# Optimization experiments

Measured on AMD Instinct MI355X. Metric: run time of the kernel, lower is better.

The kernel has to match this reference:

```python
import jax, jax.numpy as jnp
import numpy as np

H, KV, D = 12, 4, 128  # n_head, n_kv_head, head_dim
VE_GATE_CH = 12

def _rmsnorm(x):
    eps = jnp.finfo(x.dtype).eps  # matches torch F.rms_norm default eps
    return x * jax.lax.rsqrt(jnp.mean(x * x, axis=-1, keepdims=True) + eps)

def _rope(x, cos, sin):
    d = x.shape[-1] // 2
    x1, x2 = x[..., :d], x[..., d:]
    return jnp.concatenate([x1 * cos + x2 * sin, -x1 * sin + x2 * cos], axis=-1)

def setup_inputs() -> dict:
    key = jax.random.key(0)
    ks = jax.random.split(key, 9)
    B, T, C = 2, 2048, 1536
    x = jax.random.normal(ks[0], (B, T, C), jnp.float32)
    ve = jax.random.normal(ks[1], (B, T, KV * D), jnp.float32)
    ang = jax.random.uniform(ks[2], (1, T, 1, D // 2), jnp.float32) * (2.0 * np.pi)
    cos, sin = jnp.cos(ang), jnp.sin(ang)
    Wq = jax.random.normal(ks[3], (H * D, C), jnp.float32) * 0.02
    Wk = jax.random.normal(ks[4], (KV * D, C), jnp.float32) * 0.02
    Wv = jax.random.normal(ks[5], (KV * D, C), jnp.float32) * 0.02
    Wproj = jax.random.normal(ks[6], (C, C), jnp.float32) * 0.02
    Wg = jax.random.normal(ks[7], (KV, VE_GATE_CH), jnp.float32) * 0.02
    return dict(x=x, ve=ve, cos=cos, sin=sin, Wq=Wq, Wk=Wk, Wv=Wv, Wproj=Wproj, Wg=Wg, window=1024)

def reference(x, ve, cos, sin, Wq, Wk, Wv, Wproj, Wg, window):
    B, T, C = x.shape
    q = (x @ Wq.T).reshape(B, T, H, D)
    k = (x @ Wk.T).reshape(B, T, KV, D)
    v = (x @ Wv.T).reshape(B, T, KV, D)
    # value-embedding gate: 3*sigmoid(Linear(x[..., :12])) per kv head
    gate = 3.0 * jax.nn.sigmoid(x[..., :VE_GATE_CH] @ Wg.T)  # [B,T,KV]
    v = v + gate[..., None] * ve.reshape(B, T, KV, D)
    q = _rmsnorm(_rope(q, cos, sin)) * 1.2
    k = _rmsnorm(_rope(k, cos, sin)) * 1.2
    rep = H // KV  # GQA group size
    qh = q.transpose(0, 2, 1, 3).reshape(B, KV, rep, T, D)
    kh = k.transpose(0, 2, 1, 3)  # [B,KV,T,D]
    vh = v.transpose(0, 2, 1, 3)
    scores = jnp.einsum('bgrtd,bgsd->bgrts', qh, kh) / np.sqrt(D)
    row = jnp.arange(T)[:, None]
    col = jnp.arange(T)[None, :]
    if window < 0 or window >= T:
        mask = col <= row  # pure causal
    else:
        mask = (col <= row) & (row - col <= window)  # causal sliding window
    scores = jnp.where(mask, scores, -jnp.inf)
    att = jax.nn.softmax(scores, axis=-1)
    y = jnp.einsum('bgrts,bgsd->bgrtd', att, vh)
    y = y.reshape(B, H, T, D).transpose(0, 2, 1, 3).reshape(B, T, H * D)
    return y @ Wproj.T
```

## Files before the change

kernel.cpp:

```cpp
#include <hip/hip_runtime.h>
#include <hip/hip_bf16.h>
#include <math.h>

#define B_  2
#define T_  2048
#define C_  1536
#define H_  12
#define KV_ 4
#define D_  128
#define M_  (B_*T_)
#define REP_ (H_/KV_)
#define NQKV_ 2560

typedef __bf16 bf16x8 __attribute__((ext_vector_type(8)));
typedef float  f32x4  __attribute__((ext_vector_type(4)));
typedef unsigned u32x4 __attribute__((ext_vector_type(4)));

union BCast { u32x4 u; bf16x8 b; };

__device__ inline bf16x8 ldb8(const ushort* p) {
    BCast c; c.u = *reinterpret_cast<const u32x4*>(p); return c.b;
}

__device__ inline ushort f2bf(float f) {
    union { float f; unsigned u; } v; v.f = f;
    unsigned u = v.u;
    return (ushort)((u + 0x7FFF + ((u >> 16) & 1)) >> 16);
}

__device__ inline float bf2f(ushort u) {
    union { unsigned u; float f; } v; v.u = (unsigned)u << 16;
    return v.f;
}

__device__ inline void async_copy16(const ushort* g, ushort* l) {
    __builtin_amdgcn_global_load_lds(
        (const __attribute__((address_space(1))) unsigned*)g,
        (__attribute__((address_space(3))) unsigned*)l, 16, 0, 0);
}

template<bool BF16OUT>
__global__ __launch_bounds__(256) void gemm_bf16_bt(const ushort* __restrict__ A,
                                                    const ushort* __restrict__ Bm,
                                                    void* __restrict__ Cp,
                                                    int M, int N, int K) {
    __shared__ ushort As[128 * 32];
    __shared__ ushort Bs[128 * 32];
    const int tid  = threadIdx.x;
    const int wave = tid >> 6, lane = tid & 63;
    const int m16 = lane & 15, quad = lane >> 4;
    const int bm = blockIdx.y * 128, bn = blockIdx.x * 128;
    const int wm = (wave >> 1) * 64, wn = (wave & 1) * 64;

    const int lrow = lane >> 2;
    const int lcol = (lane & 3) * 8;
    const ushort* Ag = A  + (size_t)(bm + wave * 16 + lrow) * K + lcol;
    const ushort* Bg = Bm + (size_t)(bn + wave * 16 + lrow) * K + lcol;
    ushort* AsW0 = As + wave * 512;
    ushort* AsW1 = As + 2048 + wave * 512;
    ushort* BsW0 = Bs + wave * 512;
    ushort* BsW1 = Bs + 2048 + wave * 512;
    const size_t rowskip = (size_t)64 * K;

    f32x4 acc[4][4];
    #pragma unroll
    for (int i = 0; i < 4; i++)
        #pragma unroll
        for (int j = 0; j < 4; j++) acc[i][j] = (f32x4){0.f, 0.f, 0.f, 0.f};

    for (int k0 = 0; k0 < K; k0 += 32) {
        async_copy16(Ag + k0,           AsW0);
        async_copy16(Ag + k0 + rowskip, AsW1);
        async_copy16(Bg + k0,           BsW0);
        async_copy16(Bg + k0 + rowskip, BsW1);
        __syncthreads();

        bf16x8 af[4], bfr[4];
        #pragma unroll
        for (int i = 0; i < 4; i++)
            af[i] = ldb8(As + (wm + i * 16 + m16) * 32 + quad * 8);
        #pragma unroll
        for (int j = 0; j < 4; j++)
            bfr[j] = ldb8(Bs + (wn + j * 16 + m16) * 32 + quad * 8);
        #pragma unroll
        for (int i = 0; i < 4; i++)
            #pragma unroll
            for (int j = 0; j < 4; j++)
                acc[i][j] = __builtin_amdgcn_mfma_f32_16x16x32_bf16(af[i], bfr[j], acc[i][j], 0, 0, 0);
        __syncthreads();
    }

    #pragma unroll
    for (int i = 0; i < 4; i++) {
        #pragma unroll
        for (int reg = 0; reg < 4; reg++) {
            const int row = bm + wm + i * 16 + quad * 4 + reg;
            if constexpr (BF16OUT) {
                ushort* C = (ushort*)Cp;
                #pragma unroll
                for (int j = 0; j < 4; j++)
                    C[(size_t)row * N + bn + wn + j * 16 + m16] = f2bf(acc[i][j][reg]);
            } else {
                float* C = (float*)Cp;
                #pragma unroll
                for (int j = 0; j < 4; j++)
                    C[(size_t)row * N + bn + wn + j * 16 + m16] = acc[i][j][reg];
            }
        }
    }
}

#define SEG0 1572864
#define SEG1 2162688
#define SEG2 2359296
#define SEG3 2555904
#define SEG4 3145728
__global__ __launch_bounds__(256) void cast_all(const float* __restrict__ x,
                                                const float* __restrict__ Wq,
                                                const float* __restrict__ Wk,
                                                const float* __restrict__ Wv,
                                                const float* __restrict__ Wp,
                                                ushort* __restrict__ xb,
                                                ushort* __restrict__ Wqkvb,
                                                ushort* __restrict__ Wpb) {
    const int i = blockIdx.x * 256 + threadIdx.x;
    const float* src; ushort* dst; int off;
    if (i < SEG0)      { src = x;  dst = xb;                          off = 0; }
    else if (i < SEG1) { src = Wq; dst = Wqkvb;                       off = SEG0; }
    else if (i < SEG2) { src = Wk; dst = Wqkvb + (size_t)1536 * C_;   off = SEG1; }
    else if (i < SEG3) { src = Wv; dst = Wqkvb + (size_t)2048 * C_;   off = SEG2; }
    else               { src = Wp; dst = Wpb;                         off = SEG3; }
    const int j = i - off;
    float4 v = ((const float4*)src)[j];
    ((ushort4*)dst)[j] = make_ushort4(f2bf(v.x), f2bf(v.y), f2bf(v.z), f2bf(v.w));
}

__global__ __launch_bounds__(256) void rope_rms_cast(const ushort* __restrict__ qk,
                                                     ushort* __restrict__ outp,
                                                     const float* __restrict__ cosb,
                                                     const float* __restrict__ sinb,
                                                     int nh, int rowstride, int colbase,
                                                     float outscale) {
    const int idx = blockIdx.x * 4 + (threadIdx.x >> 6);
    const int bt = idx / nh;
    const int h  = idx - bt * nh;
    const int b  = bt >> 11;
    const int t  = bt & (T_ - 1);
    const ushort* p = qk + (size_t)bt * rowstride + colbase + h * D_;
    const int i = threadIdx.x & 63;
    const float x1 = bf2f(p[i]), x2 = bf2f(p[i + 64]);
    const float c = cosb[t * 64 + i], s = sinb[t * 64 + i];
    const float o1 =  x1 * c + x2 * s;
    const float o2 = -x1 * s + x2 * c;
    float ss = o1 * o1 + o2 * o2;
    #pragma unroll
    for (int off = 32; off > 0; off >>= 1) ss += __shfl_down(ss, off);
    ss = __shfl(ss, 0);
    const float scale = rsqrtf(ss * (1.0f / 128.0f) + 1.1920928955078125e-07f) * outscale;
    ushort* op = outp + ((size_t)(b * nh + h) * T_ + t) * D_;
    op[i]      = f2bf(o1 * scale);
    op[i + 64] = f2bf(o2 * scale);
}

__global__ __launch_bounds__(256) void gate_vt(const ushort* __restrict__ qkv,
                                               const float* __restrict__ x,
                                               const float* __restrict__ ve,
                                               const float* __restrict__ Wg,
                                               ushort* __restrict__ Vt) {
    const int t0 = blockIdx.x * 64, g = blockIdx.y, b = blockIdx.z;
    __shared__ float gateS[64];
    __shared__ ushort tile[128][66];
    const int tid = threadIdx.x;
    if (tid < 64) {
        const float* xr = x + (size_t)(b * T_ + t0 + tid) * C_;
        float acc = 0.f;
        #pragma unroll
        for (int c = 0; c < 12; c++) acc += xr[c] * Wg[g * 12 + c];
        gateS[tid] = 3.0f / (1.0f + __expf(-acc));
    }
    __syncthreads();
    #pragma unroll
    for (int i = 0; i < 32; i++) {
        int idx = i * 256 + tid;
        int r = idx >> 7;
        int d = idx & 127;
        size_t offv = (size_t)(b * T_ + t0 + r) * NQKV_ + 2048 + g * D_ + d;
        size_t offe = (size_t)(b * T_ + t0 + r) * 512   + g * D_ + d;
        tile[d][r] = f2bf(bf2f(qkv[offv]) + gateS[r] * ve[offe]);
    }
    __syncthreads();
    ushort* ob = Vt + ((size_t)(b * KV_ + g) * D_) * T_ + t0;
    #pragma unroll
    for (int i = 0; i < 32; i++) {
        int idx = i * 256 + tid;
        int d = idx >> 6;
        int c = idx & 63;
        ob[(size_t)d * T_ + c] = tile[d][c];
    }
}

__global__ __launch_bounds__(256, 3) void attn_mfma(const ushort* __restrict__ Qp,
                                                    const ushort* __restrict__ Kp,
                                                    const ushort* __restrict__ Vt,
                                                    ushort* __restrict__ Y,
                                                    const int* __restrict__ wptr) {
    const int t0 = blockIdx.x * 64;
    const int h  = blockIdx.y, b = blockIdx.z;
    const int g  = h / REP_;
    const int tid  = threadIdx.x;
    const int wave = tid >> 6, lane = tid & 63;
    const int m16 = lane & 15, quad = lane >> 4;

    __shared__ ushort Ks[4 * 32 * 32];
    __shared__ ushort Vs[128 * 32];
    __shared__ ushort Pl[4][16 * 40];

    const int w = *wptr;
    const bool windowed = (w >= 0 && w < T_);
    const unsigned wu = windowed ? (unsigned)w : 0x7FFFFFFFu;
    int s_lo = 0;
    if (windowed) { s_lo = t0 - w; if (s_lo < 0) s_lo = 0; }
    const int s_hi = t0 + 63;
    const int ss0 = s_lo & ~31;
    const int tw = t0 + wave * 16;

    const ushort* qrow = Qp + ((size_t)(b * H_ + h) * T_ + tw + m16) * D_ + quad * 8;
    bf16x8 qa[4];
    #pragma unroll
    for (int kc = 0; kc < 4; kc++) qa[kc] = ldb8(qrow + kc * 32);

    const ushort* kbase = Kp + (size_t)(b * KV_ + g) * T_ * D_;
    const ushort* vbase = Vt + (size_t)(b * KV_ + g) * D_ * T_;

    const int c0 = wave, c1 = wave + 4;
    const ushort* kg0 = kbase + (size_t)((c0 & 1) * 16 + (lane >> 2)) * D_ + (c0 >> 1) * 32 + (lane & 3) * 8;
    const ushort* kg1 = kbase + (size_t)((c1 & 1) * 16 + (lane >> 2)) * D_ + (c1 >> 1) * 32 + (lane & 3) * 8;
    ushort* kl0 = Ks + c0 * 512;
    ushort* kl1 = Ks + c1 * 512;
    const ushort* vg0 = vbase + (size_t)(c0 * 16 + (lane >> 2)) * T_ + (lane & 3) * 8;
    const ushort* vg1 = vbase + (size_t)(c1 * 16 + (lane >> 2)) * T_ + (lane & 3) * 8;
    ushort* vl0 = Vs + c0 * 512;
    ushort* vl1 = Vs + c1 * 512;

    f32x4 o[8];
    #pragma unroll
    for (int dt = 0; dt < 8; dt++) o[dt] = (f32x4){0.f, 0.f, 0.f, 0.f};
    f32x4 lacc = (f32x4){0.f, 0.f, 0.f, 0.f};
    BCast onesc; onesc.u = (u32x4){0x3F803F80u, 0x3F803F80u, 0x3F803F80u, 0x3F803F80u};
    const bf16x8 ones = onesc.b;
    ushort* pw = &Pl[wave][0];

    for (int ss = ss0; ss <= s_hi; ss += 32) {
        const size_t koff = (size_t)ss * D_;
        async_copy16(kg0 + koff, kl0);
        async_copy16(kg1 + koff, kl1);
        async_copy16(vg0 + ss,   vl0);
        async_copy16(vg1 + ss,   vl1);
        __syncthreads();

        f32x4 s0 = (f32x4){0.f,0.f,0.f,0.f};
        f32x4 s1 = (f32x4){0.f,0.f,0.f,0.f};
        #pragma unroll
        for (int kc = 0; kc < 4; kc++) {
            bf16x8 kf0 = ldb8(Ks + kc * 1024 + m16 * 32 + quad * 8);
            bf16x8 kf1 = ldb8(Ks + kc * 1024 + (16 + m16) * 32 + quad * 8);
            s0 = __builtin_amdgcn_mfma_f32_16x16x32_bf16(qa[kc], kf0, s0, 0, 0, 0);
            s1 = __builtin_amdgcn_mfma_f32_16x16x32_bf16(qa[kc], kf1, s1, 0, 0, 0);
        }

        const int sA = ss + m16, sB = ss + 16 + m16;
        #pragma unroll
        for (int reg = 0; reg < 4; reg++) {
            const int t = tw + quad * 4 + reg;
            const float pa = ((unsigned)(t - sA) <= wu) ? __expf(s0[reg]) : 0.f;
            const float pb = ((unsigned)(t - sB) <= wu) ? __expf(s1[reg]) : 0.f;
            pw[(quad * 4 + reg) * 40 + m16]      = f2bf(pa);
            pw[(quad * 4 + reg) * 40 + 16 + m16] = f2bf(pb);
        }

        __builtin_amdgcn_s_waitcnt(0xc07f);
        bf16x8 pfrag = ldb8(pw + m16 * 40 + quad * 8);

        #pragma unroll
        for (int dt = 0; dt < 8; dt++) {
            bf16x8 vf = ldb8(Vs + (dt * 16 + m16) * 32 + quad * 8);
            o[dt] = __builtin_amdgcn_mfma_f32_16x16x32_bf16(pfrag, vf, o[dt], 0, 0, 0);
        }
        lacc = __builtin_amdgcn_mfma_f32_16x16x32_bf16(pfrag, ones, lacc, 0, 0, 0);
        __syncthreads();
    }

    float inv[4];
    #pragma unroll
    for (int reg = 0; reg < 4; reg++) inv[reg] = 1.0f / lacc[reg];
    ushort* yb = Y + ((size_t)(b * T_ + tw + quad * 4) * H_ + h) * D_ + m16;
    #pragma unroll
    for (int reg = 0; reg < 4; reg++)
        #pragma unroll
        for (int dt = 0; dt < 8; dt++)
            yb[(size_t)reg * H_ * D_ + dt * 16] = f2bf(o[dt][reg] * inv[reg]);
}

extern "C" void kernel_launch(void* const* d_in, const int* in_sizes, int n_in,
                              void* d_out, int out_size, void* d_ws, size_t ws_size,
                              hipStream_t stream) {
    const float* x     = (const float*)d_in[0];
    const float* ve    = (const float*)d_in[1];
    const float* cosb  = (const float*)d_in[2];
    const float* sinb  = (const float*)d_in[3];
    const float* Wq    = (const float*)d_in[4];
    const float* Wk    = (const float*)d_in[5];
    const float* Wv    = (const float*)d_in[6];
    const float* Wproj = (const float*)d_in[7];
    const float* Wg    = (const float*)d_in[8];
    const int*   wptr  = (const int*)d_in[9];
    float* out = (float*)d_out;

    ushort* xb    = (ushort*)d_ws;
    ushort* qkv   = xb    + (size_t)M_ * C_;
    ushort* Qp    = qkv   + (size_t)M_ * NQKV_;
    ushort* Kp    = Qp    + (size_t)M_ * C_;
    ushort* Vt    = Kp    + (size_t)M_ * 512;
    ushort* Wqkvb = Vt    + (size_t)M_ * 512;
    ushort* Wpb   = Wqkvb + (size_t)NQKV_ * C_;

    cast_all<<<SEG4 / 256, 256, 0, stream>>>(x, Wq, Wk, Wv, Wproj, xb, Wqkvb, Wpb);

    gemm_bf16_bt<true><<<dim3(NQKV_ / 128, M_ / 128), 256, 0, stream>>>(xb, Wqkvb, qkv, M_, NQKV_, C_);

    gate_vt<<<dim3(T_ / 64, KV_, B_), 256, 0, stream>>>(qkv, x, ve, Wg, Vt);

    rope_rms_cast<<<M_ * H_ / 4, 256, 0, stream>>>(qkv, Qp, cosb, sinb, H_, NQKV_, 0,
                                                   1.2f * 1.2f * 0.08838834764831845f);
    rope_rms_cast<<<M_ * KV_ / 4, 256, 0, stream>>>(qkv, Kp, cosb, sinb, KV_, NQKV_, 1536, 1.0f);

    ushort* yb16 = qkv;
    attn_mfma<<<dim3(T_ / 64, H_, B_), 256, 0, stream>>>(Qp, Kp, Vt, yb16, wptr);

    gemm_bf16_bt<false><<<dim3(C_ / 128, M_ / 128), 256, 0, stream>>>(yb16, Wpb, out, M_, C_, C_);
}
```

Before: 285.5 us.

## Fuse RoPE and RMSNorm into QKV GEMM epilogue via permuted weight rows

```diff
diff --git a/kernel.cpp b/kernel.cpp
--- a/kernel.cpp
+++ b/kernel.cpp
@@ -37,6 +37,10 @@
     __builtin_amdgcn_global_load_lds(
         (const __attribute__((address_space(1))) unsigned*)g,
         (__attribute__((address_space(3))) unsigned*)l, 16, 0, 0);
+}
+
+__device__ __host__ inline int dperm(int d) {
+    return (d < 32) ? d : (d < 64 ? d + 32 : (d < 96 ? d - 32 : d));
 }
 
 template<bool BF16OUT>
@@ -110,11 +114,140 @@
     }
 }
 
+#define KQ_ 1536
+__global__ __launch_bounds__(256) void gemm_qkv(const ushort* __restrict__ A,
+                                                const ushort* __restrict__ Bm,
+                                                ushort* __restrict__ Qp,
+                                                ushort* __restrict__ Kp,
+                                                ushort* __restrict__ vbuf,
+                                                const float* __restrict__ cosb,
+                                                const float* __restrict__ sinb) {
+    __shared__ ushort As[128 * 32];
+    __shared__ ushort Bs[128 * 32];
+    const int tid  = threadIdx.x;
+    const int wave = tid >> 6, lane = tid & 63;
+    const int m16 = lane & 15, quad = lane >> 4;
+    const int bm = blockIdx.y * 128, bn = blockIdx.x * 128;
+    const int wm = (wave >> 1) * 64, wn = (wave & 1) * 64;
+
+    const int lrow = lane >> 2;
+    const int lcol = (lane & 3) * 8;
+    const ushort* Ag = A  + (size_t)(bm + wave * 16 + lrow) * KQ_ + lcol;
+    const ushort* Bg = Bm + (size_t)(bn + wave * 16 + lrow) * KQ_ + lcol;
+    ushort* AsW0 = As + wave * 512;
+    ushort* AsW1 = As + 2048 + wave * 512;
+    ushort* BsW0 = Bs + wave * 512;
+    ushort* BsW1 = Bs + 2048 + wave * 512;
+    const size_t rowskip = (size_t)64 * KQ_;
+
+    f32x4 acc[4][4];
+    #pragma unroll
+    for (int i = 0; i < 4; i++)
+        #pragma unroll
+        for (int j = 0; j < 4; j++) acc[i][j] = (f32x4){0.f, 0.f, 0.f, 0.f};
+
+    for (int k0 = 0; k0 < KQ_; k0 += 32) {
+        async_copy16(Ag + k0,           AsW0);
+        async_copy16(Ag + k0 + rowskip, AsW1);
+        async_copy16(Bg + k0,           BsW0);
+        async_copy16(Bg + k0 + rowskip, BsW1);
+        __syncthreads();
+
+        bf16x8 af[4], bfr[4];
+        #pragma unroll
+        for (int i = 0; i < 4; i++)
+            af[i] = ldb8(As + (wm + i * 16 + m16) * 32 + quad * 8);
+        #pragma unroll
+        for (int j = 0; j < 4; j++)
+            bfr[j] = ldb8(Bs + (wn + j * 16 + m16) * 32 + quad * 8);
+        #pragma unroll
+        for (int i = 0; i < 4; i++)
+            #pragma unroll
+            for (int j = 0; j < 4; j++)
+                acc[i][j] = __builtin_amdgcn_mfma_f32_16x16x32_bf16(af[i], bfr[j], acc[i][j], 0, 0, 0);
+        __syncthreads();
+    }
+
+    if (bn < 2048) {
+        float* ssqS = (float*)As;
+        float ssq[4][4];
+        #pragma unroll
+        for (int i = 0; i < 4; i++) {
+            #pragma unroll
+            for (int reg = 0; reg < 4; reg++) {
+                float v = acc[i][0][reg]*acc[i][0][reg] + acc[i][1][reg]*acc[i][1][reg]
+                        + acc[i][2][reg]*acc[i][2][reg] + acc[i][3][reg]*acc[i][3][reg];
+                v += __shfl_xor(v, 1); v += __shfl_xor(v, 2);
+                v += __shfl_xor(v, 4); v += __shfl_xor(v, 8);
+                ssq[i][reg] = v;
+            }
+        }
+        if (m16 == 0) {
+            #pragma unroll
+            for (int i = 0; i < 4; i++)
+                #pragma unroll
+                for (int reg = 0; reg < 4; reg++)
+                    ssqS[(wm + i*16 + quad*4 + reg) * 2 + (wave & 1)] = ssq[i][reg];
+        }
+        __syncthreads();
+
+        const bool isq = (bn < 1536);
+        const float osc = isq ? (1.2f * 1.2f * 0.08838834764831845f) : 1.0f;
+        const int hh  = isq ? (bn >> 7) : ((bn - 1536) >> 7);
+        const int nh  = isq ? H_ : KV_;
+        ushort* outp  = isq ? Qp : Kp;
+
+        float scl[4][4];
+        #pragma unroll
+        for (int i = 0; i < 4; i++) {
+            #pragma unroll
+            for (int reg = 0; reg < 4; reg++) {
+                const int r = wm + i*16 + quad*4 + reg;
+                const float tot = ssqS[r*2] + ssqS[r*2 + 1];
+                scl[i][reg] = rsqrtf(tot * (1.0f/128.0f) + 1.1920928955078125e-07f) * osc;
+            }
+        }
+
+        #pragma unroll
+        for (int i = 0; i < 4; i++) {
+            #pragma unroll
+            for (int reg = 0; reg < 4; reg++) {
+                const int row = bm + wm + i*16 + quad*4 + reg;
+                const int b = row >> 11, t = row & (T_ - 1);
+                ushort* orow = outp + ((size_t)(b * nh + hh) * T_ + t) * D_;
+                const float sc = scl[i][reg];
+                #pragma unroll
+                for (int jp = 0; jp < 2; jp++) {
+                    const int ipair = (wn ? 32 : 0) + jp*16 + m16;
+                    const float c = cosb[t*64 + ipair], s = sinb[t*64 + ipair];
+                    const float x1 = acc[i][jp][reg], x2 = acc[i][jp+2][reg];
+                    orow[wn + jp*16 + m16]       = f2bf((x1*c + x2*s) * sc);
+                    orow[wn + (jp+2)*16 + m16]   = f2bf((x2*c - x1*s) * sc);
+                }
+            }
+        }
+    } else {
+        const int cb = bn - 2048 + wn;
+        #pragma unroll
+        for (int i = 0; i < 4; i++) {
+            #pragma unroll
+            for (int reg = 0; reg < 4; reg++) {
+                const int row = bm + wm + i*16 + quad*4 + reg;
+                ushort* vr = vbuf + (size_t)row * 512 + cb + m16;
+                #pragma unroll
+                for (int j = 0; j < 4; j++)
+                    vr[j*16] = f2bf(acc[i][j][reg]);
+            }
+        }
+    }
+}
+
 #define SEG0 1572864
 #define SEG1 2162688
 #define SEG2 2359296
 #define SEG3 2555904
 #define SEG4 3145728
+#define ROW4 384
 __global__ __launch_bounds__(256) void cast_all(const float* __restrict__ x,
                                                 const float* __restrict__ Wq,
                                                 const float* __restrict__ Wk,
@@ -124,45 +257,33 @@
                                                 ushort* __restrict__ Wqkvb,
                                                 ushort* __restrict__ Wpb) {
     const int i = blockIdx.x * 256 + threadIdx.x;
-    const float* src; ushort* dst; int off;
-    if (i < SEG0)      { src = x;  dst = xb;                          off = 0; }
-    else if (i < SEG1) { src = Wq; dst = Wqkvb;                       off = SEG0; }
-    else if (i < SEG2) { src = Wk; dst = Wqkvb + (size_t)1536 * C_;   off = SEG1; }
-    else if (i < SEG3) { src = Wv; dst = Wqkvb + (size_t)2048 * C_;   off = SEG2; }
-    else               { src = Wp; dst = Wpb;                         off = SEG3; }
-    const int j = i - off;
-    float4 v = ((const float4*)src)[j];
-    ((ushort4*)dst)[j] = make_ushort4(f2bf(v.x), f2bf(v.y), f2bf(v.z), f2bf(v.w));
-}
-
-__global__ __launch_bounds__(256) void rope_rms_cast(const ushort* __restrict__ qk,
-                                                     ushort* __restrict__ outp,
-                                                     const float* __restrict__ cosb,
-                                                     const float* __restrict__ sinb,
-                                                     int nh, int rowstride, int colbase,
-                                                     float outscale) {
-    const int idx = blockIdx.x * 4 + (threadIdx.x >> 6);
-    const int bt = idx / nh;
-    const int h  = idx - bt * nh;
-    const int b  = bt >> 11;
-    const int t  = bt & (T_ - 1);
-    const ushort* p = qk + (size_t)bt * rowstride + colbase + h * D_;
-    const int i = threadIdx.x & 63;
-    const float x1 = bf2f(p[i]), x2 = bf2f(p[i + 64]);
-    const float c = cosb[t * 64 + i], s = sinb[t * 64 + i];
-    const float o1 =  x1 * c + x2 * s;
-    const float o2 = -x1 * s + x2 * c;
-    float ss = o1 * o1 + o2 * o2;
-    #pragma unroll
-    for (int off = 32; off > 0; off >>= 1) ss += __shfl_down(ss, off);
-    ss = __shfl(ss, 0);
-    const float scale = rsqrtf(ss * (1.0f / 128.0f) + 1.1920928955078125e-07f) * outscale;
-    ushort* op = outp + ((size_t)(b * nh + h) * T_ + t) * D_;
-    op[i]      = f2bf(o1 * scale);
-    op[i + 64] = f2bf(o2 * scale);
-}
-
-__global__ __launch_bounds__(256) void gate_vt(const ushort* __restrict__ qkv,
+    float4 v; size_t dst4; ushort* dstp;
+    if (i < SEG0) {
+        v = ((const float4*)x)[i]; dstp = xb; dst4 = i;
+    } else if (i < SEG1) {
+        const int j = i - SEG0;
+        const int r = j / ROW4, c4 = j - r * ROW4;
+        const int d = r & 127, hh = r >> 7;
+        v = ((const float4*)Wq)[j]; dstp = Wqkvb;
+        dst4 = (size_t)(hh * 128 + dperm(d)) * ROW4 + c4;
+    } else if (i < SEG2) {
+        const int j = i - SEG1;
+        const int r = j / ROW4, c4 = j - r * ROW4;
+        const int d = r & 127, g = r >> 7;
+        v = ((const float4*)Wk)[j]; dstp = Wqkvb;
+        dst4 = (size_t)(1536 + g * 128 + dperm(d)) * ROW4 + c4;
+    } else if (i < SEG3) {
+        const int j = i - SEG2;
+        v = ((const float4*)Wv)[j]; dstp = Wqkvb;
+        dst4 = (size_t)2048 * ROW4 + j;
+    } else {
+        const int j = i - SEG3;
+        v = ((const float4*)Wp)[j]; dstp = Wpb; dst4 = j;
+    }
+    ((ushort4*)dstp)[dst4] = make_ushort4(f2bf(v.x), f2bf(v.y), f2bf(v.z), f2bf(v.w));
+}
+
+__global__ __launch_bounds__(256) void gate_vt(const ushort* __restrict__ vbuf,
                                                const float* __restrict__ x,
                                                const float* __restrict__ ve,
                                                const float* __restrict__ Wg,
@@ -184,9 +305,8 @@
         int idx = i * 256 + tid;
         int r = idx >> 7;
         int d = idx & 127;
-        size_t offv = (size_t)(b * T_ + t0 + r) * NQKV_ + 2048 + g * D_ + d;
-        size_t offe = (size_t)(b * T_ + t0 + r) * 512   + g * D_ + d;
-        tile[d][r] = f2bf(bf2f(qkv[offv]) + gateS[r] * ve[offe]);
+        size_t offv = (size_t)(b * T_ + t0 + r) * 512 + g * D_ + d;
+        tile[d][r] = f2bf(bf2f(vbuf[offv]) + gateS[r] * ve[offv]);
     }
     __syncthreads();
     ushort* ob = Vt + ((size_t)(b * KV_ + g) * D_) * T_ + t0;
@@ -317,24 +437,21 @@
     float* out = (float*)d_out;
 
     ushort* xb    = (ushort*)d_ws;
-    ushort* qkv   = xb    + (size_t)M_ * C_;
-    ushort* Qp    = qkv   + (size_t)M_ * NQKV_;
+    ushort* vbuf  = xb    + (size_t)M_ * C_;
+    ushort* Qp    = vbuf  + (size_t)M_ * 512;
     ushort* Kp    = Qp    + (size_t)M_ * C_;
     ushort* Vt    = Kp    + (size_t)M_ * 512;
-    ushort* Wqkvb = Vt    + (size_t)M_ * 512;
+    ushort* yb16  = Vt    + (size_t)M_ * 512;
+    ushort* Wqkvb = yb16  + (size_t)M_ * C_;
     ushort* Wpb   = Wqkvb + (size_t)NQKV_ * C_;
 
     cast_all<<<SEG4 / 256, 256, 0, stream>>>(x, Wq, Wk, Wv, Wproj, xb, Wqkvb, Wpb);
 
-    gemm_bf16_bt<true><<<dim3(NQKV_ / 128, M_ / 128), 256, 0, stream>>>(xb, Wqkvb, qkv, M_, NQKV_, C_);
-
-    gate_vt<<<dim3(T_ / 64, KV_, B_), 256, 0, stream>>>(qkv, x, ve, Wg, Vt);
-
-    rope_rms_cast<<<M_ * H_ / 4, 256, 0, stream>>>(qkv, Qp, cosb, sinb, H_, NQKV_, 0,
-                                                   1.2f * 1.2f * 0.08838834764831845f);
-    rope_rms_cast<<<M_ * KV_ / 4, 256, 0, stream>>>(qkv, Kp, cosb, sinb, KV_, NQKV_, 1536, 1.0f);
-
-    ushort* yb16 = qkv;
+    gemm_qkv<<<dim3(NQKV_ / 128, M_ / 128), 256, 0, stream>>>(xb, Wqkvb, Qp, Kp, vbuf,
+                                                              cosb, sinb);
+
+    gate_vt<<<dim3(T_ / 64, KV_, B_), 256, 0, stream>>>(vbuf, x, ve, Wg, Vt);
+
     attn_mfma<<<dim3(T_ / 64, H_, B_), 256, 0, stream>>>(Qp, Kp, Vt, yb16, wptr);
 
     gemm_bf16_bt<false><<<dim3(C_ / 128, M_ / 128), 256, 0, stream>>>(yb16, Wpb, out, M_, C_, C_);
```

After: 277.5 us. 2.8% less time.
